# Optimization experiments

Hardware: AMD Instinct MI355X
Metric: run time of the kernel (lower is better)

## Reference

```python
import jax, jax.numpy as jnp
import numpy as np

N, DIN, DOUT = 8192, 4096, 4096

def setup_inputs() -> dict:
    key = jax.random.key(0)
    k1, k2 = jax.random.split(key)
    x = jax.random.normal(k1, (N, DIN), dtype=jnp.float32)
    # ternary-ish weights; forward applies sign() via STE anyway
    weight = jax.random.normal(k2, (DOUT, DIN), dtype=jnp.float32)
    bias = jnp.zeros((DOUT,), dtype=jnp.float32)
    scale = jnp.ones((1,), dtype=jnp.float32)  # scale_init = 1.0
    return {"x": x, "weight": weight, "bias": bias, "scale": scale}


def reference(x, weight, bias, scale):
    # STE sign-quantization: value is sign(weight) in {-1,0,1},
    # gradient flows to weight as identity.
    w = weight - jax.lax.stop_gradient(weight - jnp.sign(weight))
    # fused ternary matmul + scale + bias: out = scale * (x @ w.T + bias)
    # (backward in the torch code scales grad for x, w, AND bias, implying
    #  bias sits inside the scale multiplier)
    return scale[0] * (jnp.matmul(x, w.T) + bias)
```

## Files before the change

kernel.cpp:

```cpp
#include <hip/hip_runtime.h>
#include <hip/hip_bf16.h>
#include <stdint.h>

#define M_DIM 8192
#define K_DIM 4096
#define N_DIM 4096

typedef int intx4 __attribute__((ext_vector_type(4)));

__global__ void cvt_fused_i8_kernel(const float* __restrict__ x,
                                    const float* __restrict__ w,
                                    signed char* __restrict__ xb,
                                    signed char* __restrict__ wb,
                                    float* __restrict__ row_scale) {
    const int b   = blockIdx.x;
    const int tid = threadIdx.x;
    if (b < M_DIM) {
        __shared__ float wmax[4];
        const float* xr = x + (size_t)b * K_DIM;
        float4 v[4];
        const int base = tid * 16;
#pragma unroll
        for (int i = 0; i < 4; ++i) v[i] = *(const float4*)(xr + base + i * 4);

        float am = 0.f;
#pragma unroll
        for (int i = 0; i < 4; ++i) {
            am = fmaxf(am, fabsf(v[i].x)); am = fmaxf(am, fabsf(v[i].y));
            am = fmaxf(am, fabsf(v[i].z)); am = fmaxf(am, fabsf(v[i].w));
        }
#pragma unroll
        for (int off = 32; off > 0; off >>= 1)
            am = fmaxf(am, __shfl_xor(am, off));
        if ((tid & 63) == 0) wmax[tid >> 6] = am;
        __syncthreads();
        am = fmaxf(fmaxf(wmax[0], wmax[1]), fmaxf(wmax[2], wmax[3]));
        am = fmaxf(am, 1e-30f);

        const float inv = 127.f / am;
        union { signed char c[16]; uint4 u; } r;
        const float* vf = (const float*)v;
#pragma unroll
        for (int i = 0; i < 16; ++i) {
            int q = (int)rintf(vf[i] * inv);
            q = q > 127 ? 127 : (q < -127 ? -127 : q);
            r.c[i] = (signed char)q;
        }
        *(uint4*)(xb + (size_t)b * K_DIM + base) = r.u;
        if (tid == 0) row_scale[b] = am * (1.f / 127.f);
    } else {
        size_t t = ((size_t)(b - M_DIM) * blockDim.x + tid) * 8;
        float4 a = *(const float4*)(w + t);
        float4 c = *(const float4*)(w + t + 4);
        union { signed char s[8]; uint2 u; } r;
        r.s[0] = (a.x > 0.f) - (a.x < 0.f); r.s[1] = (a.y > 0.f) - (a.y < 0.f);
        r.s[2] = (a.z > 0.f) - (a.z < 0.f); r.s[3] = (a.w > 0.f) - (a.w < 0.f);
        r.s[4] = (c.x > 0.f) - (c.x < 0.f); r.s[5] = (c.y > 0.f) - (c.y < 0.f);
        r.s[6] = (c.z > 0.f) - (c.z < 0.f); r.s[7] = (c.w > 0.f) - (c.w < 0.f);
        *(uint2*)(wb + t) = r.u;
    }
}

__device__ __forceinline__ void gld_lds16(const void* g, void* l) {
    __builtin_amdgcn_global_load_lds(
        (const __attribute__((address_space(1))) void*)g,
        (__attribute__((address_space(3))) void*)l,
        16, 0, 0);
}

__global__ void __launch_bounds__(256, 4)
gemm_i8_kernel(const signed char* __restrict__ A,
               const signed char* __restrict__ B,
               const float* __restrict__ bias,
               const float* __restrict__ scale,
               const float* __restrict__ row_scale,
               float* __restrict__ out) {
    __shared__ __attribute__((aligned(16))) signed char sA[128 * 64];
    __shared__ __attribute__((aligned(16))) signed char sB[128 * 64];

    const int tid  = threadIdx.x;
    const int lane = tid & 63;
    const int wave = tid >> 6;
    const int wm = wave >> 1;
    const int wn = wave & 1;
    const int g  = lane >> 4;
    const int mn = lane & 15;

    const int rowBase = blockIdx.y * 128;
    const int colBase = blockIdx.x * 128;

    const int srow   = lane >> 2;
    const int schunk = lane & 3;
    const signed char* gA0 =
        A + (size_t)(rowBase + wave * 32 + srow) * K_DIM + schunk * 16;
    const signed char* gB0 =
        B + (size_t)(colBase + wave * 32 + srow) * K_DIM + schunk * 16;
    signed char* lA0 = &sA[(wave * 32) * 64];
    signed char* lB0 = &sB[(wave * 32) * 64];

    intx4 acc[4][4] = {};

    for (int k0 = 0; k0 < K_DIM; k0 += 64) {
        gld_lds16(gA0 + k0, lA0);
        gld_lds16(gA0 + k0 + (size_t)16 * K_DIM, lA0 + 16 * 64);
        gld_lds16(gB0 + k0, lB0);
        gld_lds16(gB0 + k0 + (size_t)16 * K_DIM, lB0 + 16 * 64);
        __syncthreads();

        intx4 af[4], bfr[4];
#pragma unroll
        for (int i = 0; i < 4; ++i)
            af[i] = *(const intx4*)(&sA[(wm * 64 + i * 16 + mn) * 64 + g * 16]);
#pragma unroll
        for (int j = 0; j < 4; ++j)
            bfr[j] = *(const intx4*)(&sB[(wn * 64 + j * 16 + mn) * 64 + g * 16]);

#pragma unroll
        for (int i = 0; i < 4; ++i)
#pragma unroll
            for (int j = 0; j < 4; ++j)
                acc[i][j] = __builtin_amdgcn_mfma_i32_16x16x64_i8(
                    af[i], bfr[j], acc[i][j], 0, 0, 0);
        __syncthreads();
    }

    const float s = scale[0];
#pragma unroll
    for (int j = 0; j < 4; ++j) {
        const int gcol = colBase + wn * 64 + j * 16 + mn;
        const float bv = bias[gcol];
#pragma unroll
        for (int i = 0; i < 4; ++i) {
            const int grow0 = rowBase + wm * 64 + i * 16 + g * 4;
            float4 rs4 = *(const float4*)(row_scale + grow0);
            float rs[4] = {rs4.x, rs4.y, rs4.z, rs4.w};
#pragma unroll
            for (int r = 0; r < 4; ++r)
                __builtin_nontemporal_store(
                    s * ((float)acc[i][j][r] * rs[r] + bv),
                    out + (size_t)(grow0 + r) * N_DIM + gcol);
        }
    }
}

__global__ void fallback_kernel(const float* __restrict__ x,
                                const float* __restrict__ w,
                                const float* __restrict__ bias,
                                const float* __restrict__ scale,
                                float* __restrict__ out) {
    int col = blockIdx.x * 64 + (threadIdx.x & 63);
    int row = blockIdx.y * 4 + (threadIdx.x >> 6);
    const float* xr = x + (size_t)row * K_DIM;
    const float* wr = w + (size_t)col * K_DIM;
    float acc = 0.f;
    for (int k = 0; k < K_DIM; k += 4) {
        float4 a = *(const float4*)(xr + k);
        float4 b = *(const float4*)(wr + k);
        acc += a.x * (b.x > 0.f ? 1.f : (b.x < 0.f ? -1.f : 0.f));
        acc += a.y * (b.y > 0.f ? 1.f : (b.y < 0.f ? -1.f : 0.f));
        acc += a.z * (b.z > 0.f ? 1.f : (b.z < 0.f ? -1.f : 0.f));
        acc += a.w * (b.w > 0.f ? 1.f : (b.w < 0.f ? -1.f : 0.f));
    }
    out[(size_t)row * N_DIM + col] = scale[0] * (acc + bias[col]);
}

extern "C" void kernel_launch(void* const* d_in, const int* in_sizes, int n_in,
                              void* d_out, int out_size, void* d_ws, size_t ws_size,
                              hipStream_t stream) {
    const float* x     = (const float*)d_in[0];
    const float* w     = (const float*)d_in[1];
    const float* bias  = (const float*)d_in[2];
    const float* scale = (const float*)d_in[3];
    float* out = (float*)d_out;

    const size_t xb_bytes = (size_t)M_DIM * K_DIM;
    const size_t wb_bytes = (size_t)N_DIM * K_DIM;
    const size_t need = xb_bytes + wb_bytes + M_DIM * sizeof(float);

    if (ws_size >= need) {
        signed char* xb = (signed char*)d_ws;
        signed char* wb = xb + xb_bytes;
        float* row_scale = (float*)(wb + wb_bytes);
        const unsigned w_blocks = (unsigned)((size_t)N_DIM * K_DIM / 8 / 256);
        cvt_fused_i8_kernel<<<dim3(M_DIM + w_blocks), 256, 0, stream>>>(
            x, w, xb, wb, row_scale);
        dim3 grid(N_DIM / 128, M_DIM / 128);
        gemm_i8_kernel<<<grid, 256, 0, stream>>>(xb, wb, bias, scale, row_scale, out);
    } else {
        dim3 grid(N_DIM / 64, M_DIM / 4);
        fallback_kernel<<<grid, 256, 0, stream>>>(x, w, bias, scale, out);
    }
}
```

Measured before the change: 416.6 us.

## Restructure int8 GEMM into 256x256 tiles with 4-stage LDS pipeline and swizzles

Rewrites the int8 MFMA GEMM to use 256x256 block tiles with 8 waves, a 4-deep shared-memory ring buffer filled by direct global-to-LDS loads issued ahead of compute, XOR-swizzled LDS layout to avoid bank conflicts, and a block-index swizzle for L2 locality. The intent is to overlap global loads with MFMA work and raise arithmetic intensity per loaded byte. The conversion kernel is also changed to coalesced strided float4 loads with 4-byte stores. The cost is 128 KB of LDS per block, which limits occupancy to one block per CU, plus fragile hand-tuned waitcnt and barrier sequencing.

```diff
diff --git a/kernel.cpp b/kernel.cpp
--- a/kernel.cpp
+++ b/kernel.cpp
@@ -19,9 +19,9 @@
         __shared__ float wmax[4];
         const float* xr = x + (size_t)b * K_DIM;
         float4 v[4];
-        const int base = tid * 16;
-#pragma unroll
-        for (int i = 0; i < 4; ++i) v[i] = *(const float4*)(xr + base + i * 4);
+#pragma unroll
+        for (int i = 0; i < 4; ++i)
+            v[i] = *(const float4*)(xr + tid * 4 + i * 1024);
 
         float am = 0.f;
 #pragma unroll
@@ -38,15 +38,18 @@
         am = fmaxf(am, 1e-30f);
 
         const float inv = 127.f / am;
-        union { signed char c[16]; uint4 u; } r;
-        const float* vf = (const float*)v;
-#pragma unroll
-        for (int i = 0; i < 16; ++i) {
-            int q = (int)rintf(vf[i] * inv);
-            q = q > 127 ? 127 : (q < -127 ? -127 : q);
-            r.c[i] = (signed char)q;
-        }
-        *(uint4*)(xb + (size_t)b * K_DIM + base) = r.u;
+#pragma unroll
+        for (int i = 0; i < 4; ++i) {
+            union { signed char c[4]; uint32_t u; } r;
+            const float* vf = (const float*)&v[i];
+#pragma unroll
+            for (int k = 0; k < 4; ++k) {
+                int q = (int)rintf(vf[k] * inv);
+                q = q > 127 ? 127 : (q < -127 ? -127 : q);
+                r.c[k] = (signed char)q;
+            }
+            *(uint32_t*)(xb + (size_t)b * K_DIM + tid * 4 + i * 1024) = r.u;
+        }
         if (tid == 0) row_scale[b] = am * (1.f / 127.f);
     } else {
         size_t t = ((size_t)(b - M_DIM) * blockDim.x + tid) * 8;
@@ -68,60 +71,116 @@
         16, 0, 0);
 }
 
-__global__ void __launch_bounds__(256, 4)
+__global__ void __launch_bounds__(512, 2)
 gemm_i8_kernel(const signed char* __restrict__ A,
                const signed char* __restrict__ B,
                const float* __restrict__ bias,
                const float* __restrict__ scale,
                const float* __restrict__ row_scale,
                float* __restrict__ out) {
-    __shared__ __attribute__((aligned(16))) signed char sA[128 * 64];
-    __shared__ __attribute__((aligned(16))) signed char sB[128 * 64];
+    __shared__ __attribute__((aligned(16))) signed char sA[4][256 * 64];
+    __shared__ __attribute__((aligned(16))) signed char sB[4][256 * 64];
 
     const int tid  = threadIdx.x;
     const int lane = tid & 63;
     const int wave = tid >> 6;
-    const int wm = wave >> 1;
-    const int wn = wave & 1;
+    const int wm = wave >> 2;
+    const int wn = wave & 3;
     const int g  = lane >> 4;
     const int mn = lane & 15;
 
-    const int rowBase = blockIdx.y * 128;
-    const int colBase = blockIdx.x * 128;
-
-    const int srow   = lane >> 2;
-    const int schunk = lane & 3;
-    const signed char* gA0 =
-        A + (size_t)(rowBase + wave * 32 + srow) * K_DIM + schunk * 16;
-    const signed char* gB0 =
-        B + (size_t)(colBase + wave * 32 + srow) * K_DIM + schunk * 16;
-    signed char* lA0 = &sA[(wave * 32) * 64];
-    signed char* lB0 = &sB[(wave * 32) * 64];
-
-    intx4 acc[4][4] = {};
-
-    for (int k0 = 0; k0 < K_DIM; k0 += 64) {
-        gld_lds16(gA0 + k0, lA0);
-        gld_lds16(gA0 + k0 + (size_t)16 * K_DIM, lA0 + 16 * 64);
-        gld_lds16(gB0 + k0, lB0);
-        gld_lds16(gB0 + k0 + (size_t)16 * K_DIM, lB0 + 16 * 64);
-        __syncthreads();
-
-        intx4 af[4], bfr[4];
-#pragma unroll
-        for (int i = 0; i < 4; ++i)
-            af[i] = *(const intx4*)(&sA[(wm * 64 + i * 16 + mn) * 64 + g * 16]);
+    const int bid = blockIdx.x;
+    const int swz = (bid & 7) * 64 + (bid >> 3);
+    const int n_idx = swz & 15;
+    const int m_idx = swz >> 4;
+    const int rowBase = m_idx * 256;
+    const int colBase = n_idx * 256;
+
+    const int sc   = (lane & 3) ^ ((lane >> 3) & 3);
+    const int srow = wave * 16 + (lane >> 2);
+    const signed char* gA0 = A + (size_t)(rowBase + srow) * K_DIM + sc * 16;
+    const signed char* gA1 = gA0 + (size_t)128 * K_DIM;
+    const signed char* gB0 = B + (size_t)(colBase + srow) * K_DIM + sc * 16;
+    const signed char* gB1 = gB0 + (size_t)128 * K_DIM;
+    const int ldsR0 = wave * 1024;
+    const int ldsR1 = 8192 + wave * 1024;
+
+    const int fxor = (g ^ ((mn >> 1) & 3)) * 16;
+    const int aoff = (wm * 128 + mn) * 64 + fxor;
+    const int boff = (wn * 64 + mn) * 64 + fxor;
+
+    intx4 acc0[4][4] = {};
+    intx4 acc1[4][4] = {};
+
+#pragma unroll
+    for (int s = 0; s < 3; ++s) {
+        const size_t kg = (size_t)s * 64;
+        gld_lds16(gA0 + kg, &sA[s][ldsR0]);
+        gld_lds16(gA1 + kg, &sA[s][ldsR1]);
+        gld_lds16(gB0 + kg, &sB[s][ldsR0]);
+        gld_lds16(gB1 + kg, &sB[s][ldsR1]);
+    }
+    asm volatile("s_waitcnt vmcnt(8)" ::: "memory");
+    __builtin_amdgcn_s_barrier();
+
+    for (int t = 0; t < 64; ++t) {
+        const signed char* sAb = sA[t & 3];
+        const signed char* sBb = sB[t & 3];
+        signed char* pA = sA[(t + 3) & 3];
+        signed char* pB = sB[(t + 3) & 3];
+        const bool stage = t < 61;
+        const size_t kg = (size_t)(t + 3) * 64;
+
+        intx4 a0[4], b0[4];
+#pragma unroll
+        for (int i = 0; i < 4; ++i)
+            a0[i] = *(const intx4*)(sAb + aoff + i * 1024);
 #pragma unroll
         for (int j = 0; j < 4; ++j)
-            bfr[j] = *(const intx4*)(&sB[(wn * 64 + j * 16 + mn) * 64 + g * 16]);
-
+            b0[j] = *(const intx4*)(sBb + boff + j * 1024);
+        if (stage) {
+            gld_lds16(gA0 + kg, pA + ldsR0);
+            gld_lds16(gA1 + kg, pA + ldsR1);
+        }
+        __builtin_amdgcn_s_barrier();
+        asm volatile("s_waitcnt lgkmcnt(0)" ::: "memory");
+        __builtin_amdgcn_sched_barrier(0);
+        __builtin_amdgcn_s_setprio(1);
 #pragma unroll
         for (int i = 0; i < 4; ++i)
 #pragma unroll
             for (int j = 0; j < 4; ++j)
-                acc[i][j] = __builtin_amdgcn_mfma_i32_16x16x64_i8(
-                    af[i], bfr[j], acc[i][j], 0, 0, 0);
-        __syncthreads();
+                acc0[i][j] = __builtin_amdgcn_mfma_i32_16x16x64_i8(
+                    a0[i], b0[j], acc0[i][j], 0, 0, 0);
+        __builtin_amdgcn_s_setprio(0);
+        __builtin_amdgcn_sched_barrier(0);
+        __builtin_amdgcn_s_barrier();
+
+        intx4 a1[4];
+#pragma unroll
+        for (int i = 0; i < 4; ++i)
+            a1[i] = *(const intx4*)(sAb + aoff + 4096 + i * 1024);
+        if (stage) {
+            gld_lds16(gB0 + kg, pB + ldsR0);
+            gld_lds16(gB1 + kg, pB + ldsR1);
+        }
+        __builtin_amdgcn_s_barrier();
+        asm volatile("s_waitcnt lgkmcnt(0)" ::: "memory");
+        __builtin_amdgcn_sched_barrier(0);
+        __builtin_amdgcn_s_setprio(1);
+#pragma unroll
+        for (int i = 0; i < 4; ++i)
+#pragma unroll
+            for (int j = 0; j < 4; ++j)
+                acc1[i][j] = __builtin_amdgcn_mfma_i32_16x16x64_i8(
+                    a1[i], b0[j], acc1[i][j], 0, 0, 0);
+        __builtin_amdgcn_s_setprio(0);
+        __builtin_amdgcn_sched_barrier(0);
+
+        if (t < 61)       asm volatile("s_waitcnt vmcnt(8)" ::: "memory");
+        else if (t == 61) asm volatile("s_waitcnt vmcnt(4)" ::: "memory");
+        else if (t == 62) asm volatile("s_waitcnt vmcnt(0)" ::: "memory");
+        __builtin_amdgcn_s_barrier();
     }
 
     const float s = scale[0];
@@ -131,14 +190,26 @@
         const float bv = bias[gcol];
 #pragma unroll
         for (int i = 0; i < 4; ++i) {
-            const int grow0 = rowBase + wm * 64 + i * 16 + g * 4;
-            float4 rs4 = *(const float4*)(row_scale + grow0);
-            float rs[4] = {rs4.x, rs4.y, rs4.z, rs4.w};
-#pragma unroll
-            for (int r = 0; r < 4; ++r)
-                __builtin_nontemporal_store(
-                    s * ((float)acc[i][j][r] * rs[r] + bv),
-                    out + (size_t)(grow0 + r) * N_DIM + gcol);
+            {
+                const int grow0 = rowBase + wm * 128 + i * 16 + g * 4;
+                const float4 rs4 = *(const float4*)(row_scale + grow0);
+                const float rs[4] = {rs4.x, rs4.y, rs4.z, rs4.w};
+#pragma unroll
+                for (int r = 0; r < 4; ++r)
+                    __builtin_nontemporal_store(
+                        s * ((float)acc0[i][j][r] * rs[r] + bv),
+                        out + (size_t)(grow0 + r) * N_DIM + gcol);
+            }
+            {
+                const int grow1 = rowBase + wm * 128 + 64 + i * 16 + g * 4;
+                const float4 rs4 = *(const float4*)(row_scale + grow1);
+                const float rs[4] = {rs4.x, rs4.y, rs4.z, rs4.w};
+#pragma unroll
+                for (int r = 0; r < 4; ++r)
+                    __builtin_nontemporal_store(
+                        s * ((float)acc1[i][j][r] * rs[r] + bv),
+                        out + (size_t)(grow1 + r) * N_DIM + gcol);
+            }
         }
     }
 }
@@ -184,8 +255,8 @@
         const unsigned w_blocks = (unsigned)((size_t)N_DIM * K_DIM / 8 / 256);
         cvt_fused_i8_kernel<<<dim3(M_DIM + w_blocks), 256, 0, stream>>>(
             x, w, xb, wb, row_scale);
-        dim3 grid(N_DIM / 128, M_DIM / 128);
-        gemm_i8_kernel<<<grid, 256, 0, stream>>>(xb, wb, bias, scale, row_scale, out);
+        gemm_i8_kernel<<<dim3((M_DIM / 256) * (N_DIM / 256)), 512, 0, stream>>>(
+            xb, wb, bias, scale, row_scale, out);
     } else {
         dim3 grid(N_DIM / 64, M_DIM / 4);
         fallback_kernel<<<grid, 256, 0, stream>>>(x, w, bias, scale, out);
```

New measurement: 419.7 us. About the same (+0.7%).
